# Kernel optimization log

Measured on AMD Instinct MI355X. Metric: run time of the kernel, lower is better.

The kernel has to match this reference:

```python
import jax, jax.numpy as jnp
import numpy as np

H = 512      # hidden_size
N = 8        # num_heads (each head has full H dims in this module)
B, T = 4, 1024
LN_EPS = 1e-5


def _layernorm(x, gamma, beta):
    mu = jnp.mean(x, axis=-1, keepdims=True)
    var = jnp.mean(jnp.square(x - mu), axis=-1, keepdims=True)
    return (x - mu) * jax.lax.rsqrt(var + LN_EPS) * gamma + beta


def setup_inputs() -> dict:
    key = jax.random.key(0)
    ks = jax.random.split(key, 8)
    s = 0.02
    return {
        "x":   jax.random.normal(ks[0], (B, T, H), dtype=jnp.float32),
        "Wq":  jax.random.normal(ks[1], (H, N * H), dtype=jnp.float32) * s,
        "Wk":  jax.random.normal(ks[2], (H, N * H), dtype=jnp.float32) * s,
        "Wv":  jax.random.normal(ks[3], (H, N * H), dtype=jnp.float32) * s,
        "Wo":  jax.random.normal(ks[4], (N * H, H), dtype=jnp.float32) * s,
        "g1":  jnp.ones((H,), jnp.float32),
        "beta1": jnp.zeros((H,), jnp.float32),
        "Wf1": jax.random.normal(ks[5], (H, 4 * H), dtype=jnp.float32) * s,
        "bf1": jnp.zeros((4 * H,), jnp.float32),
        "Wf2": jax.random.normal(ks[6], (4 * H, H), dtype=jnp.float32) * s,
        "bf2": jnp.zeros((H,), jnp.float32),
        "g2":  jnp.ones((H,), jnp.float32),
        "beta2": jnp.zeros((H,), jnp.float32),
    }


def reference(x, Wq, Wk, Wv, Wo, g1, beta1, Wf1, bf1, Wf2, bf2, g2, beta2):
    b, t, h = x.shape
    n = Wq.shape[1] // h
    # torch .view(B, N, T, H) on a contiguous (B, T, N*H) tensor is a raw
    # row-major reshape (NOT a transpose) -> identical to jnp.reshape.
    Q = (x @ Wq).reshape(b, n, t, h)
    K = (x @ Wk).reshape(b, n, t, h)
    V = (x @ Wv).reshape(b, n, t, h)
    # 'bath,bahT->batT' with K.transpose(2,3) == standard Q @ K^T per (b,a)
    logits = jnp.einsum('bath,baTh->batT', Q, K)
    attn = jax.nn.softmax(logits / (h ** 0.5), axis=-1)
    # repeated 't' in one operand takes the DIAGONAL of attn (torch semantics,
    # matched by numpy/jax einsum): h[b,a,t,:] = attn[b,a,t,t] * V[b,a,t,:]
    hh = jnp.einsum('batt,bath->bath', attn, V)
    hh = hh.reshape(b, t, n * h) @ Wo
    hh = _layernorm(x + hh, g1, beta1)
    ff = jax.nn.relu(hh @ Wf1 + bf1) @ Wf2 + bf2
    return _layernorm(hh + ff, g2, beta2)
```

## Files before the change

kernel.cpp:

```cpp
#include <hip/hip_runtime.h>
#include <stdint.h>


#define LN_EPS 1e-5f

typedef __attribute__((ext_vector_type(8))) short short8;
typedef __attribute__((ext_vector_type(4))) float f32x4;
typedef __attribute__((ext_vector_type(4))) int int4v;

__device__ __forceinline__ unsigned short f2bf(float f) {
    unsigned int u = __float_as_uint(f);
    u = (u + 0x7fffu + ((u >> 16) & 1u)) >> 16;
    return (unsigned short)u;
}
__device__ __forceinline__ float bf2f(unsigned short h) {
    return __uint_as_float(((unsigned int)h) << 16);
}
__device__ __forceinline__ signed char q8(float v, float s) {
    int q = (int)rintf(v * s);
    q = q > 127 ? 127 : (q < -127 ? -127 : q);
    return (signed char)q;
}
__device__ __forceinline__ int pperm(int w) {
    return (w & ~63) + ((w & 15) << 2) + ((w >> 4) & 3);
}

__device__ __forceinline__ void llds16(const void* g, void* l) {
    __builtin_amdgcn_global_load_lds(
        (const __attribute__((address_space(1))) void*)g,
        (__attribute__((address_space(3))) void*)l, 16, 0, 0);
}

__global__ __launch_bounds__(256) void gemm_fold(
    const unsigned short* __restrict__ A,
    const unsigned short* __restrict__ Bt,
    const unsigned short* __restrict__ A2,
    const unsigned short* __restrict__ B2,
    signed char* __restrict__ Cv,
    int N, int K, int lda, int ldb,
    long aBatch, long bBatch, long cBatch) {
    __shared__ unsigned short As[128 * 64];
    __shared__ unsigned short Bs[128 * 64];

    const int bx = blockIdx.x, by = blockIdx.y, bz = blockIdx.z;
    const int tid = threadIdx.x;
    const int wid = tid >> 6;
    const int lane = tid & 63;
    const int lr = lane & 15;
    const int kg = lane >> 4;
    const int wr = wid >> 1;
    const int wc = wid & 1;
    const int row0 = by * 128;
    const int col0 = bx * 128;

    const int zf = bz >> 3, za = bz & 7;
    const unsigned short* Ab = (zf ? A2 : A) + (long)za * aBatch;
    const unsigned short* Bb = (zf ? B2 : Bt) + (long)za * bBatch;
    const long cOff = (long)bz * cBatch;

    const int l8 = lane >> 3;
    const int cs = ((lane & 7) ^ l8) * 8;
    unsigned short* ldsA = &As[wid * 2048];
    unsigned short* ldsB = &Bs[wid * 2048];
    const unsigned short* gA = Ab + (long)(row0 + wid * 32 + l8) * lda + cs;
    const unsigned short* gB = Bb + (long)(col0 + wid * 32 + l8) * ldb + cs;

    const int lr7 = lr & 7;
    const int uS0 = ((0 + kg) ^ lr7) * 8;
    const int uS1 = ((4 + kg) ^ lr7) * 8;

    f32x4 acc[4][4];
#pragma unroll
    for (int m = 0; m < 4; ++m)
#pragma unroll
        for (int n = 0; n < 4; ++n)
#pragma unroll
            for (int j = 0; j < 4; ++j) acc[m][n][j] = 0.f;

    for (int kk = 0; kk < K; kk += 64) {
        __syncthreads();
#pragma unroll
        for (int i = 0; i < 4; ++i) {
            llds16(gA + (long)i * 8 * lda + kk, ldsA + i * 512);
            llds16(gB + (long)i * 8 * ldb + kk, ldsB + i * 512);
        }
        __syncthreads();
        short8 a[4][2], b[4][2];
#pragma unroll
        for (int m = 0; m < 4; ++m) {
            const int ro = (wr * 64 + m * 16 + lr) * 64;
            a[m][0] = *(const short8*)&As[ro + uS0];
            a[m][1] = *(const short8*)&As[ro + uS1];
        }
#pragma unroll
        for (int n = 0; n < 4; ++n) {
            const int ro = (wc * 64 + n * 16 + lr) * 64;
            b[n][0] = *(const short8*)&Bs[ro + uS0];
            b[n][1] = *(const short8*)&Bs[ro + uS1];
        }
#pragma unroll
        for (int s = 0; s < 2; ++s)
#pragma unroll
            for (int m = 0; m < 4; ++m)
#pragma unroll
                for (int n = 0; n < 4; ++n)
                    acc[m][n] = __builtin_amdgcn_mfma_f32_16x16x32_bf16(
                        a[m][s], b[n][s], acc[m][n], 0, 0, 0);
    }

    const int gbase = col0 + wc * 64 + lr * 4;
#pragma unroll
    for (int m = 0; m < 4; ++m) {
        const int grow = row0 + wr * 64 + m * 16 + kg * 4;
#pragma unroll
        for (int j = 0; j < 4; ++j) {
            unsigned int o = 0;
#pragma unroll
            for (int n = 0; n < 4; ++n)
                o |= (unsigned int)(unsigned char)q8(acc[m][n][j], 2048.f)
                     << (8 * n);
            *(unsigned int*)(Cv + cOff + (long)(grow + j) * N + gbase) = o;
        }
    }
}

template <int IM>
__global__ __launch_bounds__(256) void gemm_i8(
    const signed char* __restrict__ Abase,
    const signed char* __restrict__ Bbase,
    signed char* __restrict__ o8,
    unsigned short* __restrict__ o16,
    const float* __restrict__ bias,
    float* __restrict__ dsum, float* __restrict__ ddiag,
    float invs2048) {
    __shared__ signed char As[128 * 128];
    __shared__ signed char Bs[128 * 128];

    const int bx = blockIdx.x, by = blockIdx.y, bz = blockIdx.z;
    const int tid = threadIdx.x;
    const int wid = tid >> 6;
    const int lane = tid & 63;
    const int lr = lane & 15;
    const int kg = lane >> 4;
    const int wr = wid >> 1;
    const int wc = wid & 1;
    const int row0 = by * 128;
    const int col0 = bx * 128;

    int lda, ldb, k0 = 0;
    const signed char* Ab;
    const signed char* Bb;
    if (IM == 0) {
        lda = 512; ldb = 512;
        Ab = Abase;
        Bb = Bbase + (long)bz * (4096 * 512);
    } else if (IM == 1) {
        lda = 4096; ldb = 512;
        const int b = bz >> 3, a = bz & 7;
        Ab = Abase + (long)b * (1024 * 4096) + a * 512;
        Bb = Bbase + (long)b * (1024 * 512);
    } else if (IM == 2) {
        lda = 512; ldb = 512;
        Ab = Abase; Bb = Bbase;
    } else {
        lda = 2048; ldb = 2048;
        Ab = Abase; Bb = Bbase;
        k0 = bz * 512;
    }

    const int l8 = lane >> 3;
    const int cs = ((lane & 7) ^ l8) * 16;
    signed char* ldsA = &As[wid * 4096];
    signed char* ldsB = &Bs[wid * 4096];
    const signed char* gA = Ab + (long)(row0 + wid * 32 + l8) * lda + k0 + cs;
    const signed char* gB = Bb + (long)(col0 + wid * 32 + l8) * ldb + k0 + cs;

    const int lr7 = lr & 7;
    const int uS0 = ((0 + kg) ^ lr7) * 16;
    const int uS1 = ((4 + kg) ^ lr7) * 16;

    int4v acc[4][4];
#pragma unroll
    for (int m = 0; m < 4; ++m)
#pragma unroll
        for (int n = 0; n < 4; ++n)
#pragma unroll
            for (int j = 0; j < 4; ++j) acc[m][n][j] = 0;

    for (int kt = 0; kt < 4; ++kt) {
        const int kk = kt * 128;
        __syncthreads();
#pragma unroll
        for (int i = 0; i < 4; ++i) {
            llds16(gA + (long)i * 8 * lda + kk, ldsA + i * 1024);
            llds16(gB + (long)i * 8 * ldb + kk, ldsB + i * 1024);
        }
        __syncthreads();
        int4v av[4][2], bv[4][2];
#pragma unroll
        for (int m = 0; m < 4; ++m) {
            const int ro = (wr * 64 + m * 16 + lr) * 128;
            av[m][0] = *(const int4v*)&As[ro + uS0];
            av[m][1] = *(const int4v*)&As[ro + uS1];
        }
#pragma unroll
        for (int n = 0; n < 4; ++n) {
            const int ro = (wc * 64 + n * 16 + lr) * 128;
            bv[n][0] = *(const int4v*)&Bs[ro + uS0];
            bv[n][1] = *(const int4v*)&Bs[ro + uS1];
        }
#pragma unroll
        for (int s = 0; s < 2; ++s)
#pragma unroll
            for (int m = 0; m < 4; ++m)
#pragma unroll
                for (int n = 0; n < 4; ++n)
                    acc[m][n] = __builtin_amdgcn_mfma_i32_16x16x64_i8(
                        av[m][s], bv[n][s], acc[m][n], 0, 0, 0);
    }

    if (IM == 1) {
        const float dq = 1.52587890625e-5f;
        const int hrow0 = bz * 1024 + row0 + wr * 64;
        const bool diagblk = (bx == by) && (wr == wc);
#pragma unroll
        for (int m = 0; m < 4; ++m) {
            float es[4] = {0.f, 0.f, 0.f, 0.f};
#pragma unroll
            for (int n = 0; n < 4; ++n) {
#pragma unroll
                for (int j = 0; j < 4; ++j) {
                    const float e = __expf((float)acc[m][n][j] * dq);
                    es[j] += e;
                    if (diagblk && n == m && lr == kg * 4 + j)
                        ddiag[hrow0 + m * 16 + kg * 4 + j] = e;
                }
            }
#pragma unroll
            for (int j = 0; j < 4; ++j) {
                float s = es[j];
                s += __shfl_xor(s, 1, 64);
                s += __shfl_xor(s, 2, 64);
                s += __shfl_xor(s, 4, 64);
                s += __shfl_xor(s, 8, 64);
                if (lr == 0) atomicAdd(&dsum[hrow0 + m * 16 + kg * 4 + j], s);
            }
        }
        return;
    }

    const int gbase = col0 + wc * 64 + lr * 4;
#pragma unroll
    for (int m = 0; m < 4; ++m) {
        const int grow = row0 + wr * 64 + m * 16 + kg * 4;
#pragma unroll
        for (int j = 0; j < 4; ++j) {
            if (IM == 0) {
                unsigned int o = 0;
                const float s = (bz == 0) ? invs2048 : 128.f;
#pragma unroll
                for (int n = 0; n < 4; ++n) {
                    const float v = (float)acc[m][n][j] * 1.52587890625e-5f;
                    o |= (unsigned int)(unsigned char)q8(v, s) << (8 * n);
                }
                const long off = (bz == 0) ? 0 : (long)16777216;
                *(unsigned int*)(o8 + off + (long)(grow + j) * 4096 + gbase) = o;
            } else if (IM == 2) {
                unsigned int o = 0;
#pragma unroll
                for (int n = 0; n < 4; ++n) {
                    const int ocol = col0 + wc * 64 + n * 16 + lr;
                    const float v = fmaxf(
                        fmaf((float)acc[m][n][j], 3.0517578125e-5f,
                             bias[ocol]), 0.f);
                    o |= (unsigned int)(unsigned char)q8(v, 64.f) << (8 * n);
                }
                *(unsigned int*)(o8 + (long)(grow + j) * 2048 + gbase) = o;
            } else {
                unsigned int lo = 0, hi = 0;
                const float v0 = (float)acc[m][0][j] * 1.52587890625e-5f;
                const float v1 = (float)acc[m][1][j] * 1.52587890625e-5f;
                const float v2 = (float)acc[m][2][j] * 1.52587890625e-5f;
                const float v3 = (float)acc[m][3][j] * 1.52587890625e-5f;
                lo = (unsigned int)f2bf(v0) | ((unsigned int)f2bf(v1) << 16);
                hi = (unsigned int)f2bf(v2) | ((unsigned int)f2bf(v3) << 16);
                uint2 o; o.x = lo; o.y = hi;
                *(uint2*)(o16 + (long)bz * 2097152 + (long)(grow + j) * 512 +
                          gbase) = o;
            }
        }
    }
}

__global__ __launch_bounds__(256) void transpose_bf16(
    const float* __restrict__ src, unsigned short* __restrict__ dst,
    int R, int C) {
    __shared__ float tile[32][33];
    const int tx = threadIdx.x & 31;
    const int ty = threadIdx.x >> 5;
    const int r0 = blockIdx.y * 32;
    const int c0 = blockIdx.x * 32;
#pragma unroll
    for (int k = 0; k < 4; ++k)
        tile[ty + k * 8][tx] = src[(long)(r0 + ty + k * 8) * C + c0 + tx];
    __syncthreads();
#pragma unroll
    for (int k = 0; k < 4; ++k)
        dst[(long)(c0 + ty + k * 8) * R + r0 + tx] = f2bf(tile[tx][ty + k * 8]);
}

template <bool PERM>
__global__ __launch_bounds__(256) void transpose_i8(
    const float* __restrict__ src, signed char* __restrict__ dst,
    int R, int C) {
    __shared__ float tile[32][33];
    const int tx = threadIdx.x & 31;
    const int ty = threadIdx.x >> 5;
    const int r0 = blockIdx.y * 32;
    const int c0 = blockIdx.x * 32;
#pragma unroll
    for (int k = 0; k < 4; ++k)
        tile[ty + k * 8][tx] = src[(long)(r0 + ty + k * 8) * C + c0 + tx];
    __syncthreads();
#pragma unroll
    for (int k = 0; k < 4; ++k) {
        const int r = r0 + tx;
        const int rc = PERM ? pperm(r) : r;
        dst[(long)(c0 + ty + k * 8) * R + rc] = q8(tile[tx][ty + k * 8], 1024.f);
    }
}

__global__ __launch_bounds__(256) void convert3_bf16(
    const float* __restrict__ s0, const float* __restrict__ s1,
    const float* __restrict__ s2, unsigned short* __restrict__ dst) {
    const int idx = blockIdx.x * 256 + threadIdx.x;
    const int y = blockIdx.y;
    const float* src = (y == 0) ? s0 : (y == 1) ? s1 : s2;
    float4 a = ((const float4*)src)[idx * 2];
    float4 b = ((const float4*)src)[idx * 2 + 1];
    uint4 o;
    o.x = (unsigned int)f2bf(a.x) | ((unsigned int)f2bf(a.y) << 16);
    o.y = (unsigned int)f2bf(a.z) | ((unsigned int)f2bf(a.w) << 16);
    o.z = (unsigned int)f2bf(b.x) | ((unsigned int)f2bf(b.y) << 16);
    o.w = (unsigned int)f2bf(b.z) | ((unsigned int)f2bf(b.w) << 16);
    ((uint4*)(dst + (long)y * 2097152))[idx] = o;
}

__global__ __launch_bounds__(256) void quant_x_perm(
    const float* __restrict__ x, signed char* __restrict__ xq) {
    const int idx = blockIdx.x * 256 + threadIdx.x;
    const int t = idx >> 7;
    const int rem = idx & 127;
    const int g = rem >> 4, lr = rem & 15;
    const long rb = (long)t * 512 + g * 64;
    unsigned int o = 0;
#pragma unroll
    for (int n = 0; n < 4; ++n)
        o |= (unsigned int)(unsigned char)q8(x[rb + n * 16 + lr], 32.f)
             << (8 * n);
    *(unsigned int*)(xq + rb + lr * 4) = o;
}

__device__ __forceinline__ void ln_reduce(float v0, float v1, int tid,
                                          float* sred, float* sred2,
                                          float& mu, float& rs) {
    float sum = v0 + v1;
    float sq = v0 * v0 + v1 * v1;
#pragma unroll
    for (int off = 32; off > 0; off >>= 1) {
        sum += __shfl_down(sum, off, 64);
        sq += __shfl_down(sq, off, 64);
    }
    const int wave = tid >> 6;
    if ((tid & 63) == 0) { sred[wave] = sum; sred2[wave] = sq; }
    __syncthreads();
    if (tid == 0) {
        float s = 0.f, q = 0.f;
#pragma unroll
        for (int w = 0; w < 4; ++w) { s += sred[w]; q += sred2[w]; }
        const float m = s * (1.f / 512.f);
        const float var = q * (1.f / 512.f) - m * m;
        sred[4] = m;
        sred2[4] = rsqrtf(var + LN_EPS);
    }
    __syncthreads();
    mu = sred[4];
    rs = sred2[4];
}

__global__ __launch_bounds__(256) void ln_combine1(
    const float* __restrict__ x, const signed char* __restrict__ Uq,
    const float* __restrict__ dsum, const float* __restrict__ ddiag,
    const float* __restrict__ g, const float* __restrict__ be,
    float* __restrict__ y1, signed char* __restrict__ y1q) {
    __shared__ float sred[8], sred2[8], df[8];
    const int row = blockIdx.x;
    const int tid = threadIdx.x;
    if (tid < 8) {
        const int b = row >> 10, t = row & 1023;
        const int idx = (b * 8 + tid) * 1024 + t;
        df[tid] = ddiag[idx] / dsum[idx] * (1.f / 128.f);
    }
    __syncthreads();
    const long base = (long)row * 512;
    const long ubase = (long)row * 4096;
    const int p0 = pperm(tid);
    const int p1 = pperm(tid + 256);
    float v0 = x[base + tid];
    float v1 = x[base + tid + 256];
#pragma unroll
    for (int a = 0; a < 8; ++a) {
        const float d = df[a];
        const long ub = ubase + a * 512;
        v0 = fmaf(d, (float)Uq[ub + p0], v0);
        v1 = fmaf(d, (float)Uq[ub + p1], v1);
    }
    float mu, rs;
    ln_reduce(v0, v1, tid, sred, sred2, mu, rs);
    const float o0 = (v0 - mu) * rs * g[tid] + be[tid];
    const float o1 = (v1 - mu) * rs * g[tid + 256] + be[tid + 256];
    y1[base + tid] = o0;
    y1[base + tid + 256] = o1;
    y1q[base + tid] = q8(o0, 32.f);
    y1q[base + tid + 256] = q8(o1, 32.f);
}

__global__ __launch_bounds__(256) void ln_combine2(
    const float* __restrict__ y1, const unsigned short* __restrict__ ffp,
    const float* __restrict__ bias, const float* __restrict__ g,
    const float* __restrict__ be, float* __restrict__ out) {
    __shared__ float sred[8], sred2[8];
    const int row = blockIdx.x;
    const int tid = threadIdx.x;
    const long base = (long)row * 512;
    const int p0 = pperm(tid);
    const int p1 = pperm(tid + 256);
    float v0 = y1[base + tid] + bias[tid];
    float v1 = y1[base + tid + 256] + bias[tid + 256];
#pragma unroll
    for (int z = 0; z < 4; ++z) {
        const long fb = (long)z * 2097152 + base;
        v0 += bf2f(ffp[fb + p0]);
        v1 += bf2f(ffp[fb + p1]);
    }
    float mu, rs;
    ln_reduce(v0, v1, tid, sred, sred2, mu, rs);
    out[base + tid] = (v0 - mu) * rs * g[tid] + be[tid];
    out[base + tid + 256] = (v1 - mu) * rs * g[tid + 256] + be[tid + 256];
}

extern "C" void kernel_launch(void* const* d_in, const int* in_sizes, int n_in,
                              void* d_out, int out_size, void* d_ws, size_t ws_size,
                              hipStream_t stream) {
    const float* x     = (const float*)d_in[0];
    const float* Wq    = (const float*)d_in[1];
    const float* Wk    = (const float*)d_in[2];
    const float* Wv    = (const float*)d_in[3];
    const float* Wo    = (const float*)d_in[4];
    const float* g1    = (const float*)d_in[5];
    const float* beta1 = (const float*)d_in[6];
    const float* Wf1   = (const float*)d_in[7];
    const float* bf1   = (const float*)d_in[8];
    const float* Wf2   = (const float*)d_in[9];
    const float* bf2   = (const float*)d_in[10];
    const float* g2    = (const float*)d_in[11];
    const float* beta2 = (const float*)d_in[12];
    float* out = (float*)d_out;

    char* p = (char*)d_ws;
    unsigned short* Wqb  = (unsigned short*)p; p += (long)512 * 4096 * 2;
    unsigned short* Wkb  = (unsigned short*)p; p += (long)512 * 4096 * 2;
    unsigned short* Wvb  = (unsigned short*)p; p += (long)512 * 4096 * 2;
    unsigned short* WoT  = (unsigned short*)p; p += (long)512 * 4096 * 2;
    signed char*  Wf1Tq  = (signed char*)p;    p += (long)2048 * 512;
    signed char*  Wf2Tq  = (signed char*)p;    p += (long)512 * 2048;
    signed char*  Wallq8 = (signed char*)p;    p += (long)8192 * 512;
    signed char*  PUq8   = (signed char*)p;    p += (long)2 * 4096 * 4096;
    signed char*  xq8    = (signed char*)p;    p += (long)4096 * 512;
    signed char*  y1q8   = (signed char*)p;    p += (long)4096 * 512;
    signed char*  f1q8   = (signed char*)p;    p += (long)4096 * 2048;
    float* dsum  = (float*)p; p += (long)32768 * 4;
    float* ddiag = (float*)p; p += (long)32768 * 4;
    float* y1    = (float*)p; p += (long)4096 * 512 * 4;
    unsigned short* ffp = (unsigned short*)p; p += (long)4 * 4096 * 512 * 2;

    const dim3 blk(256);
    const float invs = 0.04419417382415922f;

    convert3_bf16<<<dim3(1024, 3), blk, 0, stream>>>(Wq, Wk, Wv, Wqb);
    quant_x_perm<<<dim3(2048), blk, 0, stream>>>(x, xq8);
    transpose_bf16<<<dim3(512 / 32, 4096 / 32), blk, 0, stream>>>(Wo, WoT, 4096, 512);
    transpose_i8<false><<<dim3(2048 / 32, 512 / 32), blk, 0, stream>>>(Wf1, Wf1Tq, 512, 2048);
    transpose_i8<true><<<dim3(512 / 32, 2048 / 32), blk, 0, stream>>>(Wf2, Wf2Tq, 2048, 512);
    hipMemsetAsync(dsum, 0, 32768 * sizeof(float), stream);

    gemm_fold<<<dim3(4, 4, 16), blk, 0, stream>>>(
        Wkb, Wqb, WoT, Wvb, Wallq8,
        512, 512, 4096, 4096, 512, 512, (long)512 * 512);

    gemm_i8<0><<<dim3(32, 32, 2), blk, 0, stream>>>(
        xq8, Wallq8, PUq8, nullptr, nullptr, nullptr, nullptr, invs * 2048.f);

    gemm_i8<1><<<dim3(8, 8, 32), blk, 0, stream>>>(
        PUq8, xq8, nullptr, nullptr, nullptr, dsum, ddiag, 0.f);

    ln_combine1<<<dim3(4096), blk, 0, stream>>>(
        x, PUq8 + (long)16777216, dsum, ddiag, g1, beta1, y1, y1q8);

    gemm_i8<2><<<dim3(16, 32, 1), blk, 0, stream>>>(
        y1q8, Wf1Tq, f1q8, nullptr, bf1, nullptr, nullptr, 0.f);

    gemm_i8<3><<<dim3(4, 32, 4), blk, 0, stream>>>(
        f1q8, Wf2Tq, nullptr, ffp, nullptr, nullptr, nullptr, 0.f);

    ln_combine2<<<dim3(4096), blk, 0, stream>>>(y1, ffp, bf2, g2, beta2, out);
}
```

Measured before the change: 131.1 us.

## Use 256-wide K tiles in int8 GEMM and remap workgroups across XCDs

The int8 GEMM now stages 256-byte K slices into shared memory, so each tile needs two iterations instead of four, halving the number of barrier pairs. The global-to-LDS load pattern and swizzle are reworked to match the wider rows. The flat block index is also permuted so that consecutive workgroups land on the same XCD, which should improve L2 reuse. The cost is doubled LDS use (64KB per block), which may lower occupancy, and the remap assumes the block count divides evenly by 8.

```diff
diff --git a/kernel.cpp b/kernel.cpp
--- a/kernel.cpp
+++ b/kernel.cpp
@@ -133,10 +133,17 @@
     const float* __restrict__ bias,
     float* __restrict__ dsum, float* __restrict__ ddiag,
     float invs2048) {
-    __shared__ signed char As[128 * 128];
-    __shared__ signed char Bs[128 * 128];
-
-    const int bx = blockIdx.x, by = blockIdx.y, bz = blockIdx.z;
+    __shared__ signed char As[128 * 256];
+    __shared__ signed char Bs[128 * 256];
+
+    const unsigned gx = gridDim.x, gy = gridDim.y;
+    const unsigned nwg = gx * gy * gridDim.z;
+    unsigned flat = blockIdx.x + gx * (blockIdx.y + gy * blockIdx.z);
+    flat = (flat & 7u) * (nwg >> 3) + (flat >> 3);
+    const int bx = flat % gx;
+    const int by = (flat / gx) % gy;
+    const int bz = flat / (gx * gy);
+
     const int tid = threadIdx.x;
     const int wid = tid >> 6;
     const int lane = tid & 63;
@@ -168,12 +175,10 @@
         k0 = bz * 512;
     }
 
-    const int l8 = lane >> 3;
-    const int cs = ((lane & 7) ^ l8) * 16;
-    signed char* ldsA = &As[wid * 4096];
-    signed char* ldsB = &Bs[wid * 4096];
-    const signed char* gA = Ab + (long)(row0 + wid * 32 + l8) * lda + k0 + cs;
-    const signed char* gB = Bb + (long)(col0 + wid * 32 + l8) * ldb + k0 + cs;
+    const int rl4 = lane >> 4;
+    const int sw0 = (((lane & 7) ^ rl4) * 16) + (((lane >> 3) & 1) * 128);
+    const signed char* gA0 = Ab + (long)(row0 + rl4) * lda + k0;
+    const signed char* gB0 = Bb + (long)(col0 + rl4) * ldb + k0;
 
     const int lr7 = lr & 7;
     const int uS0 = ((0 + kg) ^ lr7) * 16;
@@ -187,36 +192,44 @@
 #pragma unroll
             for (int j = 0; j < 4; ++j) acc[m][n][j] = 0;
 
-    for (int kt = 0; kt < 4; ++kt) {
-        const int kk = kt * 128;
+    for (int kt = 0; kt < 2; ++kt) {
+        const int kk = kt * 256;
         __syncthreads();
 #pragma unroll
-        for (int i = 0; i < 4; ++i) {
-            llds16(gA + (long)i * 8 * lda + kk, ldsA + i * 1024);
-            llds16(gB + (long)i * 8 * ldb + kk, ldsB + i * 1024);
+        for (int i = 0; i < 8; ++i) {
+            const int sw = sw0 ^ ((i & 1) << 6);
+            const int rb = wid * 32 + i * 4;
+            llds16(gA0 + (long)(rb - rl4 + rl4) * 0 + (long)(i * 4) * lda +
+                       (long)(wid * 32) * lda + kk + sw,
+                   As + rb * 256);
+            llds16(gB0 + (long)(i * 4) * ldb + (long)(wid * 32) * ldb + kk + sw,
+                   Bs + rb * 256);
         }
         __syncthreads();
-        int4v av[4][2], bv[4][2];
-#pragma unroll
-        for (int m = 0; m < 4; ++m) {
-            const int ro = (wr * 64 + m * 16 + lr) * 128;
-            av[m][0] = *(const int4v*)&As[ro + uS0];
-            av[m][1] = *(const int4v*)&As[ro + uS1];
-        }
-#pragma unroll
-        for (int n = 0; n < 4; ++n) {
-            const int ro = (wc * 64 + n * 16 + lr) * 128;
-            bv[n][0] = *(const int4v*)&Bs[ro + uS0];
-            bv[n][1] = *(const int4v*)&Bs[ro + uS1];
-        }
-#pragma unroll
-        for (int s = 0; s < 2; ++s)
-#pragma unroll
-            for (int m = 0; m < 4; ++m)
-#pragma unroll
-                for (int n = 0; n < 4; ++n)
-                    acc[m][n] = __builtin_amdgcn_mfma_i32_16x16x64_i8(
-                        av[m][s], bv[n][s], acc[m][n], 0, 0, 0);
+#pragma unroll
+        for (int h = 0; h < 2; ++h) {
+            int4v av[4][2], bv[4][2];
+#pragma unroll
+            for (int m = 0; m < 4; ++m) {
+                const int ro = (wr * 64 + m * 16 + lr) * 256 + h * 128;
+                av[m][0] = *(const int4v*)&As[ro + uS0];
+                av[m][1] = *(const int4v*)&As[ro + uS1];
+            }
+#pragma unroll
+            for (int n = 0; n < 4; ++n) {
+                const int ro = (wc * 64 + n * 16 + lr) * 256 + h * 128;
+                bv[n][0] = *(const int4v*)&Bs[ro + uS0];
+                bv[n][1] = *(const int4v*)&Bs[ro + uS1];
+            }
+#pragma unroll
+            for (int s = 0; s < 2; ++s)
+#pragma unroll
+                for (int m = 0; m < 4; ++m)
+#pragma unroll
+                    for (int n = 0; n < 4; ++n)
+                        acc[m][n] = __builtin_amdgcn_mfma_i32_16x16x64_i8(
+                            av[m][s], bv[n][s], acc[m][n], 0, 0, 0);
+        }
     }
 
     if (IM == 1) {
@@ -277,14 +290,13 @@
                 }
                 *(unsigned int*)(o8 + (long)(grow + j) * 2048 + gbase) = o;
             } else {
-                unsigned int lo = 0, hi = 0;
                 const float v0 = (float)acc[m][0][j] * 1.52587890625e-5f;
                 const float v1 = (float)acc[m][1][j] * 1.52587890625e-5f;
                 const float v2 = (float)acc[m][2][j] * 1.52587890625e-5f;
                 const float v3 = (float)acc[m][3][j] * 1.52587890625e-5f;
-                lo = (unsigned int)f2bf(v0) | ((unsigned int)f2bf(v1) << 16);
-                hi = (unsigned int)f2bf(v2) | ((unsigned int)f2bf(v3) << 16);
-                uint2 o; o.x = lo; o.y = hi;
+                uint2 o;
+                o.x = (unsigned int)f2bf(v0) | ((unsigned int)f2bf(v1) << 16);
+                o.y = (unsigned int)f2bf(v2) | ((unsigned int)f2bf(v3) << 16);
                 *(uint2*)(o16 + (long)bz * 2097152 + (long)(grow + j) * 512 +
                           gbase) = o;
             }
```

Result: slower. 143.2 us (+9.2%).
